# Kernel tuning notes

Hardware: AMD Instinct MI355X
Metric: run time of the kernel (lower is better)

Reference implementation:

```python
import jax, jax.numpy as jnp
import numpy as np

USER = 50000
ITEM = 20000
N = USER + ITEM
LATDIM = 64
GNN_LAYERS = 2
LAM = 0.2  # args.ris_adj_lambda
IMG_DIM = 4096
TXT_DIM = 768
E_MAIN = 2_000_000
E_MODAL = 1_000_000


def setup_inputs() -> dict:
    key = jax.random.key(0)
    ks = jax.random.split(key, 25)
    f32 = jnp.float32
    inp = {
        "image_embedding": jax.random.normal(ks[0], (ITEM, IMG_DIM), f32),
        "text_embedding": jax.random.normal(ks[1], (ITEM, TXT_DIM), f32),
        "adj_rows": jax.random.randint(ks[2], (E_MAIN,), 0, N, jnp.int32),
        "adj_cols": jax.random.randint(ks[3], (E_MAIN,), 0, N, jnp.int32),
        "adj_vals": jax.random.uniform(ks[4], (E_MAIN,), f32),
        "img_rows": jax.random.randint(ks[5], (E_MODAL,), 0, N, jnp.int32),
        "img_cols": jax.random.randint(ks[6], (E_MODAL,), 0, N, jnp.int32),
        "img_vals": jax.random.uniform(ks[7], (E_MODAL,), f32),
        "txt_rows": jax.random.randint(ks[8], (E_MODAL,), 0, N, jnp.int32),
        "txt_cols": jax.random.randint(ks[9], (E_MODAL,), 0, N, jnp.int32),
        "txt_vals": jax.random.uniform(ks[10], (E_MODAL,), f32),
        "u_sh": jax.random.normal(ks[11], (USER, LATDIM), f32) * 0.1,
        "i_sh": jax.random.normal(ks[12], (ITEM, LATDIM), f32) * 0.1,
        "Wi_sh": jax.random.normal(ks[13], (IMG_DIM, LATDIM), f32) * 0.02,
        "bi_sh": jnp.zeros((LATDIM,), f32),
        "Wt_sh": jax.random.normal(ks[14], (TXT_DIM, LATDIM), f32) * 0.02,
        "bt_sh": jnp.zeros((LATDIM,), f32),
        "u_vsp": jax.random.normal(ks[15], (USER, LATDIM), f32) * 0.1,
        "i_vsp": jax.random.normal(ks[16], (ITEM, LATDIM), f32) * 0.1,
        "Wi_vsp": jax.random.normal(ks[17], (IMG_DIM, LATDIM), f32) * 0.02,
        "bi_vsp": jnp.zeros((LATDIM,), f32),
        "u_tsp": jax.random.normal(ks[18], (USER, LATDIM), f32) * 0.1,
        "i_tsp": jax.random.normal(ks[19], (ITEM, LATDIM), f32) * 0.1,
        "Wt_tsp": jax.random.normal(ks[20], (TXT_DIM, LATDIM), f32) * 0.02,
        "bt_tsp": jnp.zeros((LATDIM,), f32),
    }
    return inp


def _spmm(rows, cols, vals, x):
    # sparse COO [N,N] @ dense [N,D]: gather source rows, scale, scatter-add to dest rows
    return jax.ops.segment_sum(vals[:, None] * x[cols], rows, num_segments=N)


def _l2norm(x):
    # F.normalize(x, p=2, dim=1), eps=1e-12
    n = jnp.linalg.norm(x, axis=1, keepdims=True)
    return x / jnp.maximum(n, 1e-12)


def _branch(uE, iE, feats, ar, ac, av, mr, mc, mv):
    base = jnp.concatenate([uE, iE], axis=0)
    e_adj = _spmm(mr, mc, mv, base)                                   # modal graph aggregation
    e = _spmm(ar, ac, av, jnp.concatenate([uE, _l2norm(feats)], 0))   # pass 1: normalized modal feats
    e2 = _spmm(ar, ac, av, jnp.concatenate([e[:USER], iE], 0))        # pass 2: propagated users + id emb
    e = e + e2 + LAM * e_adj
    total = e
    cur = e
    for _ in range(GNN_LAYERS):
        cur = _spmm(ar, ac, av, cur)
        total = total + cur
    return total  # [N, LATDIM]


def reference(image_embedding, text_embedding,
              adj_rows, adj_cols, adj_vals,
              img_rows, img_cols, img_vals,
              txt_rows, txt_cols, txt_vals,
              u_sh, i_sh, Wi_sh, bi_sh, Wt_sh, bt_sh,
              u_vsp, i_vsp, Wi_vsp, bi_vsp,
              u_tsp, i_tsp, Wt_tsp, bt_tsp):
    # trans == 1: Linear feature projections
    img_sh = image_embedding @ Wi_sh + bi_sh
    txt_sh = text_embedding @ Wt_sh + bt_sh
    # shared-modal model (Model_modal_sh.forward_MM)
    ev_sh = _branch(u_sh, i_sh, img_sh, adj_rows, adj_cols, adj_vals, img_rows, img_cols, img_vals)
    et_sh = _branch(u_sh, i_sh, txt_sh, adj_rows, adj_cols, adj_vals, txt_rows, txt_cols, txt_vals)
    sh = jnp.concatenate([ev_sh, et_sh], axis=-1)  # [N, 2*LATDIM]
    # visual-specific model (Model_visual_sp.forward_MM)
    img_sp = image_embedding @ Wi_vsp + bi_vsp
    ev_sp = _branch(u_vsp, i_vsp, img_sp, adj_rows, adj_cols, adj_vals, img_rows, img_cols, img_vals)
    # text-specific model (Model_text_sp.forward_MM)
    txt_sp = text_embedding @ Wt_tsp + bt_tsp
    et_sp = _branch(u_tsp, i_tsp, txt_sp, adj_rows, adj_cols, adj_vals, txt_rows, txt_cols, txt_vals)
    # pack all model outputs into one array: [N, 4*LATDIM]
    return jnp.concatenate([sh, ev_sp, et_sp], axis=-1)
```

## Files before the change

### kernel.cpp

```cpp
#include <hip/hip_runtime.h>

#define USERN 50000
#define ITEMN 20000
#define NN    70000
#define DTOT  256
#define LAMv  0.2f
#define E_MAINN  2000000
#define E_MODALN 1000000
#define SCAN_NBLK 35

typedef float  v4f  __attribute__((ext_vector_type(4)));
typedef float  v8f  __attribute__((ext_vector_type(8)));
typedef short  v8s  __attribute__((ext_vector_type(8)));
typedef unsigned short v8u __attribute__((ext_vector_type(8)));

__device__ inline unsigned short f2bf(float f) {
    unsigned u = __float_as_uint(f);
    u += 0x7FFFu + ((u >> 16) & 1u);
    return (unsigned short)(u >> 16);
}
__device__ inline v8f bf8f(v8u u) {
    v8f f;
    #pragma unroll
    for (int i = 0; i < 8; ++i) f[i] = __uint_as_float((unsigned)u[i] << 16);
    return f;
}
__device__ inline v8u f8bf(v8f f) {
    v8u u;
    #pragma unroll
    for (int i = 0; i < 8; ++i) u[i] = f2bf(f[i]);
    return u;
}
__device__ inline ushort4 f4bf(float4 f) {
    return make_ushort4(f2bf(f.x), f2bf(f.y), f2bf(f.z), f2bf(f.w));
}

__global__ __launch_bounds__(256) void wt_build(
    const float* __restrict__ W0, const float* __restrict__ W1, int K,
    unsigned short* __restrict__ Wtb)
{
    int idx = blockIdx.x * 256 + threadIdx.x;
    if (idx >= 128 * K) return;
    int c = idx / K, k = idx - c * K;
    float v = (c < 64) ? W0[(size_t)k * 64 + c] : W1[(size_t)k * 64 + (c - 64)];
    Wtb[idx] = f2bf(v);
}

#define LDK 40

__global__ __launch_bounds__(256) void gemm_mfma(
    const float* __restrict__ A, int M, int K,
    const unsigned short* __restrict__ Wtb,
    float* __restrict__ P, int blkA, int blkB)
{
    __shared__ __align__(16) unsigned short As[64 * LDK];
    __shared__ __align__(16) unsigned short Ws[128 * LDK];
    const int tid  = threadIdx.x;
    const int row0 = blockIdx.x * 64;
    const int segLen = K >> 1;
    const int k0   = blockIdx.y * segLen;
    const int kend = k0 + segLen;
    float* outP = P + (size_t)blockIdx.y * ITEMN * DTOT;

    const int w   = tid >> 6;
    const int l   = tid & 63;
    const int l16 = l & 15, kg = l >> 4;

    const int sar = tid >> 2, sak = (tid & 3) * 8;
    const int swc = tid >> 1, swk = (tid & 1) * 16;

    v4f acc[8];
    #pragma unroll
    for (int n = 0; n < 8; ++n) acc[n] = (v4f)0.f;

    for (int kt = k0; kt < kend; kt += 32) {
        __syncthreads();
        {
            int arow = row0 + sar; if (arow >= M) arow = M - 1;
            const float* ap = A + (size_t)arow * K + kt + sak;
            float4 a0 = ((const float4*)ap)[0];
            float4 a1 = ((const float4*)ap)[1];
            *(ushort4*)&As[sar * LDK + sak]     = f4bf(a0);
            *(ushort4*)&As[sar * LDK + sak + 4] = f4bf(a1);
            const unsigned short* wp = Wtb + (size_t)swc * K + kt + swk;
            *(uint4*)&Ws[swc * LDK + swk]     = ((const uint4*)wp)[0];
            *(uint4*)&Ws[swc * LDK + swk + 8] = ((const uint4*)wp)[1];
        }
        __syncthreads();

        v8s af = *(const v8s*)&As[(w * 16 + l16) * LDK + kg * 8];
        #pragma unroll
        for (int n = 0; n < 8; ++n) {
            v8s bf = *(const v8s*)&Ws[(n * 16 + l16) * LDK + kg * 8];
            acc[n] = __builtin_amdgcn_mfma_f32_16x16x32_bf16(af, bf, acc[n], 0, 0, 0);
        }
    }

    #pragma unroll
    for (int n = 0; n < 8; ++n) {
        const int col  = n * 16 + l16;
        const int gcol = (col < 64) ? blkA * 64 + col : blkB * 64 + (col - 64);
        #pragma unroll
        for (int r = 0; r < 4; ++r) {
            int row = row0 + w * 16 + kg * 4 + r;
            if (row < M) outP[(size_t)row * DTOT + gcol] = acc[n][r];
        }
    }
}

__global__ __launch_bounds__(256) void build_feats(
    const float* __restrict__ P,
    const float* __restrict__ u_sh, const float* __restrict__ u_vsp, const float* __restrict__ u_tsp,
    const float* __restrict__ i_sh, const float* __restrict__ i_vsp, const float* __restrict__ i_tsp,
    const float* __restrict__ bi_sh, const float* __restrict__ bt_sh,
    const float* __restrict__ bi_vsp, const float* __restrict__ bt_tsp,
    unsigned short* __restrict__ X1b, unsigned short* __restrict__ X2b)
{
    const int n = blockIdx.x;
    const int t = threadIdx.x;
    const int b = t >> 6, k = t & 63;
    if (n < USERN) {
        const float* u = (b < 2) ? u_sh : (b == 2 ? u_vsp : u_tsp);
        X1b[(size_t)n * DTOT + t] = f2bf(u[(size_t)n * 64 + k]);
    } else {
        const int it = n - USERN;
        const size_t SEG = (size_t)ITEMN * DTOT;
        size_t idx = (size_t)it * DTOT + t;
        float f = P[idx] + P[idx + SEG];
        const float* bias = (b == 0) ? bi_sh : (b == 1 ? bt_sh : (b == 2 ? bi_vsp : bt_tsp));
        f += bias[k];
        float s = f * f;
        #pragma unroll
        for (int off = 32; off > 0; off >>= 1) s += __shfl_xor(s, off, 64);
        X1b[(size_t)n * DTOT + t] = f2bf(f / fmaxf(sqrtf(s), 1e-12f));
        const float* p = (b < 2) ? i_sh : (b == 2 ? i_vsp : i_tsp);
        X2b[(size_t)n * DTOT + t] = f2bf(p[(size_t)it * 64 + k]);
    }
}

__global__ __launch_bounds__(256) void hist3(
    const int* __restrict__ ar, const int* __restrict__ mir, const int* __restrict__ mtr,
    int* __restrict__ cntA, int* __restrict__ cntI, int* __restrict__ cntT)
{
    const int total = E_MAINN + 2 * E_MODALN;
    for (int i = blockIdx.x * blockDim.x + threadIdx.x; i < total; i += gridDim.x * blockDim.x) {
        if (i < E_MAINN)                    atomicAdd(&cntA[ar[i]], 1);
        else if (i < E_MAINN + E_MODALN)    atomicAdd(&cntI[mir[i - E_MAINN]], 1);
        else                                atomicAdd(&cntT[mtr[i - E_MAINN - E_MODALN]], 1);
    }
}

__device__ inline int wave_incl_scan64(int x, int lane) {
    #pragma unroll
    for (int off = 1; off < 64; off <<= 1) {
        int t = __shfl_up(x, off, 64);
        if (lane >= off) x += t;
    }
    return x;
}

__global__ __launch_bounds__(1024) void scan_bsum(
    const int* __restrict__ cntA, const int* __restrict__ cntI, const int* __restrict__ cntT,
    int* __restrict__ partial)
{
    const int g = blockIdx.y;
    const int* cnt = (g == 0) ? cntA : (g == 1 ? cntI : cntT);
    int i0 = blockIdx.x * 2048 + threadIdx.x;
    int i1 = i0 + 1024;
    int v = ((i0 < NN) ? cnt[i0] : 0) + ((i1 < NN) ? cnt[i1] : 0);
    __shared__ int ws[16];
    const int lane = threadIdx.x & 63, wv = threadIdx.x >> 6;
    #pragma unroll
    for (int off = 32; off > 0; off >>= 1) v += __shfl_xor(v, off, 64);
    if (lane == 0) ws[wv] = v;
    __syncthreads();
    if (threadIdx.x == 0) {
        int s = 0;
        #pragma unroll
        for (int i = 0; i < 16; ++i) s += ws[i];
        partial[g * SCAN_NBLK + blockIdx.x] = s;
    }
}

__global__ __launch_bounds__(1024) void scan_write(
    const int* __restrict__ cntA, const int* __restrict__ cntI, const int* __restrict__ cntT,
    const int* __restrict__ partial,
    int* __restrict__ rpA, int* __restrict__ rpI, int* __restrict__ rpT)
{
    const int g = blockIdx.y;
    const int* cnt = (g == 0) ? cntA : (g == 1 ? cntI : cntT);
    int* rp        = (g == 0) ? rpA  : (g == 1 ? rpI  : rpT);
    __shared__ int sbase;
    __shared__ int wsum[16];
    const int tid = threadIdx.x, lane = tid & 63, wv = tid >> 6;
    if (tid == 0) {
        int s = 0;
        for (int i = 0; i < (int)blockIdx.x; ++i) s += partial[g * SCAN_NBLK + i];
        sbase = s;
    }
    __syncthreads();
    int run = sbase;
    const int base = blockIdx.x * 2048;
    #pragma unroll
    for (int c = 0; c < 2; ++c) {
        int i = base + c * 1024 + tid;
        int v = (i < NN) ? cnt[i] : 0;
        int x = wave_incl_scan64(v, lane);
        if (lane == 63) wsum[wv] = x;
        __syncthreads();
        if (wv == 0 && lane < 16) {
            int s = wsum[lane];
            #pragma unroll
            for (int off = 1; off < 16; off <<= 1) {
                int t = __shfl_up(s, off, 64);
                if (lane >= off) s += t;
            }
            wsum[lane] = s;
        }
        __syncthreads();
        int woff = (wv > 0) ? wsum[wv - 1] : 0;
        if (i < NN)       rp[i]  = run + woff + x - v;
        else if (i == NN) rp[NN] = run + woff + x;
        run += wsum[15];
        __syncthreads();
    }
}

__global__ __launch_bounds__(256) void scatter3(
    const int* __restrict__ ar,  const int* __restrict__ ac,  const float* __restrict__ av,
    const int* __restrict__ mir, const int* __restrict__ mic, const float* __restrict__ miv,
    const int* __restrict__ mtr, const int* __restrict__ mtc, const float* __restrict__ mtv,
    const int* __restrict__ rpA, const int* __restrict__ rpI, const int* __restrict__ rpT,
    int* __restrict__ cntA, int* __restrict__ cntI, int* __restrict__ cntT,
    uint2* __restrict__ evA, uint2* __restrict__ evI, uint2* __restrict__ evT)
{
    const int total = E_MAINN + 2 * E_MODALN;
    for (int i = blockIdx.x * blockDim.x + threadIdx.x; i < total; i += gridDim.x * blockDim.x) {
        if (i < E_MAINN) {
            int r = ar[i];
            int pos = rpA[r] + atomicSub(&cntA[r], 1) - 1;
            evA[pos] = make_uint2((unsigned)ac[i], __float_as_uint(av[i]));
        } else if (i < E_MAINN + E_MODALN) {
            int e = i - E_MAINN;
            int r = mir[e];
            int pos = rpI[r] + atomicSub(&cntI[r], 1) - 1;
            evI[pos] = make_uint2((unsigned)mic[e], __float_as_uint(miv[e]));
        } else {
            int e = i - E_MAINN - E_MODALN;
            int r = mtr[e];
            int pos = rpT[r] + atomicSub(&cntT[r], 1) - 1;
            evT[pos] = make_uint2((unsigned)mtc[e], __float_as_uint(mtv[e]));
        }
    }
}

#define SPMM8_HEAD                                                                  \
    const int w = (blockIdx.x * blockDim.x + threadIdx.x) >> 6;                     \
    if (w >= NN) return;                                                            \
    const int lane = threadIdx.x & 63;                                              \
    const int half = lane >> 5, l5 = lane & 31;                                     \
    const v8u* __restrict__ Xv = (const v8u*)Xb;                                    \
    int e = rp[w]; const int end = rp[w + 1];                                       \
    v8f acc = (v8f)0.f;                                                             \
    for (; e + 8 <= end; e += 8) {                                                  \
        uint2 q0 = ev[e + half],     q1 = ev[e + 2 + half];                         \
        uint2 q2 = ev[e + 4 + half], q3 = ev[e + 6 + half];                         \
        v8f g0 = bf8f(Xv[(size_t)q0.x * 32 + l5]);                                  \
        v8f g1 = bf8f(Xv[(size_t)q1.x * 32 + l5]);                                  \
        v8f g2 = bf8f(Xv[(size_t)q2.x * 32 + l5]);                                  \
        v8f g3 = bf8f(Xv[(size_t)q3.x * 32 + l5]);                                  \
        float v0 = __uint_as_float(q0.y), v1 = __uint_as_float(q1.y);               \
        float v2 = __uint_as_float(q2.y), v3 = __uint_as_float(q3.y);               \
        _Pragma("unroll")                                                           \
        for (int i = 0; i < 8; ++i) {                                               \
            acc[i] = fmaf(v0, g0[i], acc[i]); acc[i] = fmaf(v1, g1[i], acc[i]);     \
            acc[i] = fmaf(v2, g2[i], acc[i]); acc[i] = fmaf(v3, g3[i], acc[i]);     \
        }                                                                           \
    }                                                                               \
    for (; e + 2 <= end; e += 2) {                                                  \
        uint2 q = ev[e + half];                                                     \
        v8f g = bf8f(Xv[(size_t)q.x * 32 + l5]);                                    \
        float v = __uint_as_float(q.y);                                             \
        _Pragma("unroll")                                                           \
        for (int i = 0; i < 8; ++i) acc[i] = fmaf(v, g[i], acc[i]);                 \
    }                                                                               \
    if (e < end && half == 0) {                                                     \
        uint2 q = ev[e];                                                            \
        v8f g = bf8f(Xv[(size_t)q.x * 32 + l5]);                                    \
        float v = __uint_as_float(q.y);                                             \
        _Pragma("unroll")                                                           \
        for (int i = 0; i < 8; ++i) acc[i] = fmaf(v, g[i], acc[i]);                 \
    }                                                                               \
    _Pragma("unroll")                                                               \
    for (int i = 0; i < 8; ++i) acc[i] += __shfl_xor(acc[i], 32, 64);               \
    if (half != 0) return;                                                          \
    const size_t oidx = (size_t)w * DTOT + l5 * 8;

__global__ __launch_bounds__(256) void spmm_e1(
    const int* __restrict__ rp, const uint2* __restrict__ ev,
    const unsigned short* __restrict__ Xb, float* __restrict__ E1,
    unsigned short* __restrict__ X2b)
{
    SPMM8_HEAD
    *(v8f*)&E1[oidx] = acc;
    if (w < USERN) *(v8u*)&X2b[oidx] = f8bf(acc);
}

__global__ __launch_bounds__(256) void fused_comb_main(
    const int* __restrict__ rp, const uint2* __restrict__ ev,
    const unsigned short* __restrict__ Xb, const float* __restrict__ E1, float* __restrict__ out)
{
    SPMM8_HEAD
    v8f o = *(const v8f*)&E1[oidx];
    #pragma unroll
    for (int i = 0; i < 8; ++i) o[i] += acc[i];
    *(v8f*)&out[oidx] = o;
}

__global__ __launch_bounds__(256) void spmm_l1(
    const int* __restrict__ rp, const uint2* __restrict__ ev,
    const unsigned short* __restrict__ Xb, float* __restrict__ C1, unsigned short* __restrict__ C1b)
{
    SPMM8_HEAD
    *(v8f*)&C1[oidx] = acc;
    *(v8u*)&C1b[oidx] = f8bf(acc);
}

__global__ __launch_bounds__(256) void fused_final(
    const int* __restrict__ rp, const uint2* __restrict__ ev,
    const unsigned short* __restrict__ Xb, const float* __restrict__ C1f, float* __restrict__ out)
{
    SPMM8_HEAD
    v8f o = *(const v8f*)&out[oidx];
    v8f c = *(const v8f*)&C1f[oidx];
    #pragma unroll
    for (int i = 0; i < 8; ++i) o[i] += c[i] + acc[i];
    *(v8f*)&out[oidx] = o;
}

__global__ __launch_bounds__(256) void modal_add(
    const int* __restrict__ rpI, const uint2* __restrict__ evI,
    const int* __restrict__ rpT, const uint2* __restrict__ evT,
    const unsigned short* __restrict__ X1b, const unsigned short* __restrict__ X2b,
    float* __restrict__ out, unsigned short* __restrict__ OUTb)
{
    const int gw = (blockIdx.x * blockDim.x + threadIdx.x) >> 6;
    if (gw >= 2 * NN) return;
    const int r = gw >> 1, m = gw & 1;
    const int lane = threadIdx.x & 63;
    const int qt = lane >> 4, l4 = lane & 15;
    const int* rp   = m ? rpT : rpI;
    const uint2* ev = m ? evT : evI;
    const int slot = m * 8 + (l4 >> 3) * 16 + (l4 & 7);
    const v8u* X1v = (const v8u*)X1b;
    const v8u* X2v = (const v8u*)X2b;
    v8f acc = (v8f)0.f;
    int e = rp[r]; const int end = rp[r + 1];
    for (; e + 4 <= end; e += 4) {
        uint2 q = ev[e + qt];
        const v8u* B = ((int)q.x < USERN) ? X1v : X2v;
        v8f g = bf8f(B[(size_t)q.x * 32 + slot]);
        float v = __uint_as_float(q.y) * LAMv;
        #pragma unroll
        for (int i = 0; i < 8; ++i) acc[i] = fmaf(v, g[i], acc[i]);
    }
    if (qt < end - e) {
        uint2 q = ev[e + qt];
        const v8u* B = ((int)q.x < USERN) ? X1v : X2v;
        v8f g = bf8f(B[(size_t)q.x * 32 + slot]);
        float v = __uint_as_float(q.y) * LAMv;
        #pragma unroll
        for (int i = 0; i < 8; ++i) acc[i] = fmaf(v, g[i], acc[i]);
    }
    #pragma unroll
    for (int i = 0; i < 8; ++i) {
        acc[i] += __shfl_xor(acc[i], 16, 64);
        acc[i] += __shfl_xor(acc[i], 32, 64);
    }
    if (lane < 16) {
        const size_t idx = (size_t)r * DTOT + slot * 8;
        v8f o = *(const v8f*)&out[idx];
        #pragma unroll
        for (int i = 0; i < 8; ++i) o[i] += acc[i];
        *(v8f*)&out[idx] = o;
        *(v8u*)&OUTb[idx] = f8bf(o);
    }
}

extern "C" void kernel_launch(void* const* d_in, const int* in_sizes, int n_in,
                              void* d_out, int out_size, void* d_ws, size_t ws_size,
                              hipStream_t stream)
{
    const float* img = (const float*)d_in[0];
    const float* txt = (const float*)d_in[1];
    const int*   ar  = (const int*)d_in[2];
    const int*   ac  = (const int*)d_in[3];
    const float* av  = (const float*)d_in[4];
    const int*   mir = (const int*)d_in[5];
    const int*   mic = (const int*)d_in[6];
    const float* miv = (const float*)d_in[7];
    const int*   mtr = (const int*)d_in[8];
    const int*   mtc = (const int*)d_in[9];
    const float* mtv = (const float*)d_in[10];
    const float* u_sh   = (const float*)d_in[11];
    const float* i_sh   = (const float*)d_in[12];
    const float* Wi_sh  = (const float*)d_in[13];
    const float* bi_sh  = (const float*)d_in[14];
    const float* Wt_sh  = (const float*)d_in[15];
    const float* bt_sh  = (const float*)d_in[16];
    const float* u_vsp  = (const float*)d_in[17];
    const float* i_vsp  = (const float*)d_in[18];
    const float* Wi_vsp = (const float*)d_in[19];
    const float* bi_vsp = (const float*)d_in[20];
    const float* u_tsp  = (const float*)d_in[21];
    const float* i_tsp  = (const float*)d_in[22];
    const float* Wt_tsp = (const float*)d_in[23];
    const float* bt_tsp = (const float*)d_in[24];

    const size_t NE = (size_t)NN * DTOT;
    float*  E1   = (float*)d_ws;
    float*  C1   = E1 + NE;
    unsigned short* X1b  = (unsigned short*)(C1 + NE);
    unsigned short* X2b  = X1b + NE;
    unsigned short* OUTb = X2b + NE;
    unsigned short* C1b  = X1b;
    unsigned short* WtbI = OUTb + NE;
    unsigned short* WtbT = WtbI + 128 * 4096;
    int*   rpA   = (int*)(WtbT + 128 * 768);
    int*   rpI   = rpA + (NN + 4);
    int*   rpT   = rpI + (NN + 4);
    int*   cntA  = rpT + (NN + 4);
    int*   cntI  = cntA + NN;
    int*   cntT  = cntI + NN;
    int*   partial = cntT + NN;
    uint2* evA   = (uint2*)(partial + 3 * SCAN_NBLK + 1);
    uint2* evI   = evA + E_MAINN;
    uint2* evT   = evI + E_MODALN;
    float* P     = E1;
    float* out   = (float*)d_out;

    const int waveBlocks  = (NN * 64) / 256;
    const int modalBlocks = (2 * NN * 64) / 256;

    hipMemsetAsync(cntA, 0, 3 * (size_t)NN * sizeof(int), stream);
    hist3<<<2048, 256, 0, stream>>>(ar, mir, mtr, cntA, cntI, cntT);
    scan_bsum<<<dim3(SCAN_NBLK, 3), 1024, 0, stream>>>(cntA, cntI, cntT, partial);
    scan_write<<<dim3(SCAN_NBLK, 3), 1024, 0, stream>>>(cntA, cntI, cntT, partial, rpA, rpI, rpT);
    scatter3<<<2048, 256, 0, stream>>>(ar, ac, av, mir, mic, miv, mtr, mtc, mtv,
                                       rpA, rpI, rpT, cntA, cntI, cntT, evA, evI, evT);

    wt_build<<<(128 * 4096 + 255) / 256, 256, 0, stream>>>(Wi_sh, Wi_vsp, 4096, WtbI);
    wt_build<<<(128 * 768  + 255) / 256, 256, 0, stream>>>(Wt_sh, Wt_tsp,  768, WtbT);

    gemm_mfma<<<dim3((ITEMN + 63) / 64, 2), 256, 0, stream>>>(img, ITEMN, 4096, WtbI, P, 0, 2);
    gemm_mfma<<<dim3((ITEMN + 63) / 64, 2), 256, 0, stream>>>(txt, ITEMN,  768, WtbT, P, 1, 3);

    build_feats<<<NN, 256, 0, stream>>>(P, u_sh, u_vsp, u_tsp, i_sh, i_vsp, i_tsp,
                                        bi_sh, bt_sh, bi_vsp, bt_tsp, X1b, X2b);

    spmm_e1<<<waveBlocks, 256, 0, stream>>>(rpA, evA, X1b, E1, X2b);

    fused_comb_main<<<waveBlocks, 256, 0, stream>>>(rpA, evA, X2b, E1, out);

    modal_add<<<modalBlocks, 256, 0, stream>>>(rpI, evI, rpT, evT, X1b, X2b, out, OUTb);

    spmm_l1<<<waveBlocks, 256, 0, stream>>>(rpA, evA, OUTb, C1, C1b);

    fused_final<<<waveBlocks, 256, 0, stream>>>(rpA, evA, C1b, C1, out);
}
```

Measured before the change: 1.271 ms.

## Two-pass bucketed CSR build and bf16 intermediates for SpMM layers

Replaces the per-row atomic scatter with a two-pass partition. Edges are first bucketed into groups of 16 rows, with the local row packed into the high bits of the column index, and a per-bucket block then does the final placement using shared-memory atomics. This is meant to improve write locality and cut contention on global atomics. It also stores the E1 and C1 intermediates in bf16 instead of fp32, halving their traffic, and fused_final reads C1 from the bf16 buffer it already uses for gathering. The cost is an extra pass over the edges, more workspace, and some precision loss in the E1 and C1 terms.

```diff
diff --git a/kernel.cpp b/kernel.cpp
--- a/kernel.cpp
+++ b/kernel.cpp
@@ -8,6 +8,8 @@
 #define E_MAINN  2000000
 #define E_MODALN 1000000
 #define SCAN_NBLK 35
+#define R0BITS 4
+#define NBUCK  (NN >> R0BITS)
 
 typedef float  v4f  __attribute__((ext_vector_type(4)));
 typedef float  v8f  __attribute__((ext_vector_type(8)));
@@ -226,31 +228,57 @@
     }
 }
 
-__global__ __launch_bounds__(256) void scatter3(
+__global__ __launch_bounds__(256) void partition3(
     const int* __restrict__ ar,  const int* __restrict__ ac,  const float* __restrict__ av,
     const int* __restrict__ mir, const int* __restrict__ mic, const float* __restrict__ miv,
     const int* __restrict__ mtr, const int* __restrict__ mtc, const float* __restrict__ mtv,
     const int* __restrict__ rpA, const int* __restrict__ rpI, const int* __restrict__ rpT,
-    int* __restrict__ cntA, int* __restrict__ cntI, int* __restrict__ cntT,
-    uint2* __restrict__ evA, uint2* __restrict__ evI, uint2* __restrict__ evT)
+    int* __restrict__ bcnt,
+    uint2* __restrict__ tmpA, uint2* __restrict__ tmpI, uint2* __restrict__ tmpT)
 {
     const int total = E_MAINN + 2 * E_MODALN;
     for (int i = blockIdx.x * blockDim.x + threadIdx.x; i < total; i += gridDim.x * blockDim.x) {
         if (i < E_MAINN) {
-            int r = ar[i];
-            int pos = rpA[r] + atomicSub(&cntA[r], 1) - 1;
-            evA[pos] = make_uint2((unsigned)ac[i], __float_as_uint(av[i]));
+            int r = ar[i], b = r >> R0BITS;
+            int pos = rpA[b << R0BITS] + atomicAdd(&bcnt[b], 1);
+            tmpA[pos] = make_uint2(((unsigned)(r & 15) << 17) | (unsigned)ac[i], __float_as_uint(av[i]));
         } else if (i < E_MAINN + E_MODALN) {
             int e = i - E_MAINN;
-            int r = mir[e];
-            int pos = rpI[r] + atomicSub(&cntI[r], 1) - 1;
-            evI[pos] = make_uint2((unsigned)mic[e], __float_as_uint(miv[e]));
+            int r = mir[e], b = r >> R0BITS;
+            int pos = rpI[b << R0BITS] + atomicAdd(&bcnt[NBUCK + b], 1);
+            tmpI[pos] = make_uint2(((unsigned)(r & 15) << 17) | (unsigned)mic[e], __float_as_uint(miv[e]));
         } else {
             int e = i - E_MAINN - E_MODALN;
-            int r = mtr[e];
-            int pos = rpT[r] + atomicSub(&cntT[r], 1) - 1;
-            evT[pos] = make_uint2((unsigned)mtc[e], __float_as_uint(mtv[e]));
+            int r = mtr[e], b = r >> R0BITS;
+            int pos = rpT[b << R0BITS] + atomicAdd(&bcnt[2 * NBUCK + b], 1);
+            tmpT[pos] = make_uint2(((unsigned)(r & 15) << 17) | (unsigned)mtc[e], __float_as_uint(mtv[e]));
         }
+    }
+}
+
+__global__ __launch_bounds__(256) void local_scatter(
+    const int* __restrict__ rpA, const int* __restrict__ rpI, const int* __restrict__ rpT,
+    const uint2* __restrict__ tmpA, const uint2* __restrict__ tmpI, const uint2* __restrict__ tmpT,
+    uint2* __restrict__ evA, uint2* __restrict__ evI, uint2* __restrict__ evT)
+{
+    const int g = blockIdx.y;
+    const int* rp     = (g == 0) ? rpA  : (g == 1 ? rpI  : rpT);
+    const uint2* tmp  = (g == 0) ? tmpA : (g == 1 ? tmpI : tmpT);
+    uint2* ev         = (g == 0) ? evA  : (g == 1 ? evI  : evT);
+    const int r0 = blockIdx.x << R0BITS;
+    __shared__ int lrp[17];
+    __shared__ int lcnt[16];
+    const int tid = threadIdx.x;
+    if (tid < 17) lrp[tid] = rp[r0 + tid];
+    if (tid < 16) lcnt[tid] = 0;
+    __syncthreads();
+    const int base = lrp[0];
+    const int count = lrp[16] - base;
+    for (int t = tid; t < count; t += 256) {
+        uint2 q = tmp[base + t];
+        int rl = q.x >> 17;
+        int k = atomicAdd(&lcnt[rl], 1);
+        ev[lrp[rl] + k] = make_uint2(q.x & 0x1FFFFu, q.y);
     }
 }
 
@@ -298,20 +326,22 @@
 
 __global__ __launch_bounds__(256) void spmm_e1(
     const int* __restrict__ rp, const uint2* __restrict__ ev,
-    const unsigned short* __restrict__ Xb, float* __restrict__ E1,
+    const unsigned short* __restrict__ Xb, unsigned short* __restrict__ E1b,
     unsigned short* __restrict__ X2b)
 {
     SPMM8_HEAD
-    *(v8f*)&E1[oidx] = acc;
-    if (w < USERN) *(v8u*)&X2b[oidx] = f8bf(acc);
+    v8u ub = f8bf(acc);
+    *(v8u*)&E1b[oidx] = ub;
+    if (w < USERN) *(v8u*)&X2b[oidx] = ub;
 }
 
 __global__ __launch_bounds__(256) void fused_comb_main(
     const int* __restrict__ rp, const uint2* __restrict__ ev,
-    const unsigned short* __restrict__ Xb, const float* __restrict__ E1, float* __restrict__ out)
+    const unsigned short* __restrict__ Xb, const unsigned short* __restrict__ E1b,
+    float* __restrict__ out)
 {
     SPMM8_HEAD
-    v8f o = *(const v8f*)&E1[oidx];
+    v8f o = bf8f(*(const v8u*)&E1b[oidx]);
     #pragma unroll
     for (int i = 0; i < 8; ++i) o[i] += acc[i];
     *(v8f*)&out[oidx] = o;
@@ -319,20 +349,19 @@
 
 __global__ __launch_bounds__(256) void spmm_l1(
     const int* __restrict__ rp, const uint2* __restrict__ ev,
-    const unsigned short* __restrict__ Xb, float* __restrict__ C1, unsigned short* __restrict__ C1b)
+    const unsigned short* __restrict__ Xb, unsigned short* __restrict__ C1b)
 {
     SPMM8_HEAD
-    *(v8f*)&C1[oidx] = acc;
     *(v8u*)&C1b[oidx] = f8bf(acc);
 }
 
 __global__ __launch_bounds__(256) void fused_final(
     const int* __restrict__ rp, const uint2* __restrict__ ev,
-    const unsigned short* __restrict__ Xb, const float* __restrict__ C1f, float* __restrict__ out)
+    const unsigned short* __restrict__ Xb, float* __restrict__ out)
 {
     SPMM8_HEAD
     v8f o = *(const v8f*)&out[oidx];
-    v8f c = *(const v8f*)&C1f[oidx];
+    v8f c = bf8f(Xv[(size_t)w * 32 + l5]);
     #pragma unroll
     for (int i = 0; i < 8; ++i) o[i] += c[i] + acc[i];
     *(v8f*)&out[oidx] = o;
@@ -418,36 +447,40 @@
     const float* bt_tsp = (const float*)d_in[24];
 
     const size_t NE = (size_t)NN * DTOT;
-    float*  E1   = (float*)d_ws;
-    float*  C1   = E1 + NE;
-    unsigned short* X1b  = (unsigned short*)(C1 + NE);
+    unsigned short* X1b  = (unsigned short*)d_ws;
     unsigned short* X2b  = X1b + NE;
     unsigned short* OUTb = X2b + NE;
+    unsigned short* E1b  = OUTb + NE;
     unsigned short* C1b  = X1b;
-    unsigned short* WtbI = OUTb + NE;
+    float* P = (float*)(E1b + NE);
+    unsigned short* WtbI = (unsigned short*)(P + 2 * (size_t)ITEMN * DTOT);
     unsigned short* WtbT = WtbI + 128 * 4096;
-    int*   rpA   = (int*)(WtbT + 128 * 768);
+    uint2* evA  = (uint2*)(WtbT + 128 * 768);
+    uint2* evI  = evA + E_MAINN;
+    uint2* evT  = evI + E_MODALN;
+    uint2* tmpA = evT + E_MODALN;
+    uint2* tmpI = tmpA + E_MAINN;
+    uint2* tmpT = tmpI + E_MODALN;
+    int*   rpA   = (int*)(tmpT + E_MODALN);
     int*   rpI   = rpA + (NN + 4);
     int*   rpT   = rpI + (NN + 4);
     int*   cntA  = rpT + (NN + 4);
     int*   cntI  = cntA + NN;
     int*   cntT  = cntI + NN;
-    int*   partial = cntT + NN;
-    uint2* evA   = (uint2*)(partial + 3 * SCAN_NBLK + 1);
-    uint2* evI   = evA + E_MAINN;
-    uint2* evT   = evI + E_MODALN;
-    float* P     = E1;
+    int*   bcnt  = cntT + NN;
+    int*   partial = bcnt + 3 * NBUCK;
     float* out   = (float*)d_out;
 
     const int waveBlocks  = (NN * 64) / 256;
     const int modalBlocks = (2 * NN * 64) / 256;
 
-    hipMemsetAsync(cntA, 0, 3 * (size_t)NN * sizeof(int), stream);
+    hipMemsetAsync(cntA, 0, (3 * (size_t)NN + 3 * NBUCK) * sizeof(int), stream);
     hist3<<<2048, 256, 0, stream>>>(ar, mir, mtr, cntA, cntI, cntT);
     scan_bsum<<<dim3(SCAN_NBLK, 3), 1024, 0, stream>>>(cntA, cntI, cntT, partial);
     scan_write<<<dim3(SCAN_NBLK, 3), 1024, 0, stream>>>(cntA, cntI, cntT, partial, rpA, rpI, rpT);
-    scatter3<<<2048, 256, 0, stream>>>(ar, ac, av, mir, mic, miv, mtr, mtc, mtv,
-                                       rpA, rpI, rpT, cntA, cntI, cntT, evA, evI, evT);
+    partition3<<<2048, 256, 0, stream>>>(ar, ac, av, mir, mic, miv, mtr, mtc, mtv,
+                                         rpA, rpI, rpT, bcnt, tmpA, tmpI, tmpT);
+    local_scatter<<<dim3(NBUCK, 3), 256, 0, stream>>>(rpA, rpI, rpT, tmpA, tmpI, tmpT, evA, evI, evT);
 
     wt_build<<<(128 * 4096 + 255) / 256, 256, 0, stream>>>(Wi_sh, Wi_vsp, 4096, WtbI);
     wt_build<<<(128 * 768  + 255) / 256, 256, 0, stream>>>(Wt_sh, Wt_tsp,  768, WtbT);
@@ -458,13 +491,13 @@
     build_feats<<<NN, 256, 0, stream>>>(P, u_sh, u_vsp, u_tsp, i_sh, i_vsp, i_tsp,
                                         bi_sh, bt_sh, bi_vsp, bt_tsp, X1b, X2b);
 
-    spmm_e1<<<waveBlocks, 256, 0, stream>>>(rpA, evA, X1b, E1, X2b);
-
-    fused_comb_main<<<waveBlocks, 256, 0, stream>>>(rpA, evA, X2b, E1, out);
+    spmm_e1<<<waveBlocks, 256, 0, stream>>>(rpA, evA, X1b, E1b, X2b);
+
+    fused_comb_main<<<waveBlocks, 256, 0, stream>>>(rpA, evA, X2b, E1b, out);
 
     modal_add<<<modalBlocks, 256, 0, stream>>>(rpI, evI, rpT, evT, X1b, X2b, out, OUTb);
 
-    spmm_l1<<<waveBlocks, 256, 0, stream>>>(rpA, evA, OUTb, C1, C1b);
-
-    fused_final<<<waveBlocks, 256, 0, stream>>>(rpA, evA, C1b, C1, out);
-}
+    spmm_l1<<<waveBlocks, 256, 0, stream>>>(rpA, evA, OUTb, C1b);
+
+    fused_final<<<waveBlocks, 256, 0, stream>>>(rpA, evA, C1b, out);
+}
```

Measured after the change: 1.272 ms. Within noise of the previous version (+0.1%).
